# Performance work log

Hardware: AMD Instinct MI355X
Metric: run time of the kernel (lower is better)

The kernel has to match this reference:

```python
import jax, jax.numpy as jnp
import numpy as np

H = 1024
S = 32768

def setup_inputs() -> dict:
    key = jax.random.key(0)
    k1, k2, k3, k4 = jax.random.split(key, 4)
    hidden = jax.random.normal(k1, (H,), dtype=jnp.float32)
    encoder_outputs = jax.random.normal(k2, (S, H), dtype=jnp.float32)
    W = jax.random.normal(k3, (H, H), dtype=jnp.float32) * (1.0 / np.sqrt(H))
    b = jax.random.normal(k4, (H,), dtype=jnp.float32) * 0.01
    return {"hidden": hidden, "encoder_outputs": encoder_outputs, "W": W, "b": b}

def reference(hidden, encoder_outputs, W, b):
    # energy_i = dot(hidden, W @ enc_i + b); vectorized over the seq dim.
    # [S,H] @ [H,H]^T -> [S,H]; then contract with hidden -> [S]
    energies = jnp.einsum('sh,h->s', encoder_outputs @ W.T + b, hidden)
    attn = jax.nn.softmax(energies)  # softmax over seq_len (dim 0), as in F.softmax
    return attn[None, None, :]  # [1, 1, S]
```

## Files before the change

### kernel.cpp

```cpp
#include <hip/hip_runtime.h>
#include <math.h>


#define H 1024
#define S 32768

__global__ __launch_bounds__(256) void k1_v_partial(const float* __restrict__ W,
                                                    const float* __restrict__ h,
                                                    float* __restrict__ partial_v) {
    __shared__ float lds[128];
    int ic   = blockIdx.x >> 3;
    int tile = blockIdx.x & 7;
    int t    = threadIdx.x;
    int c    = tile * 128 + (t & 127);
    int par  = t >> 7;
    int j0   = ic * 64 + par;
    float acc = 0.f;
    #pragma unroll 8
    for (int i = 0; i < 32; ++i) {
        int j = j0 + 2 * i;
        acc = fmaf(W[(size_t)j * H + c], h[j], acc);
    }
    if (par) lds[t - 128] = acc;
    __syncthreads();
    if (!par) partial_v[ic * H + c] = acc + lds[t];
}

__global__ __launch_bounds__(256) void k1b_v_reduce(const float* __restrict__ partial_v,
                                                    float* __restrict__ v) {
    int k = blockIdx.x * 256 + threadIdx.x;
    float acc = 0.f;
    #pragma unroll
    for (int ic = 0; ic < 16; ++ic)
        acc += partial_v[ic * H + k];
    v[k] = acc;
}

__global__ __launch_bounds__(256) void k2_energies(const float* __restrict__ E,
                                                   const float* __restrict__ v,
                                                   float* __restrict__ energies,
                                                   float* __restrict__ bmax) {
    __shared__ float vl[H];
    __shared__ float red[8];
    int t = threadIdx.x;

    ((float4*)vl)[t] = ((const float4*)v)[t];
    __syncthreads();

    int wave = t >> 6, lane = t & 63;
    size_t row0 = (size_t)blockIdx.x * 8 + wave * 2;
    const float4* e0 = (const float4*)(E + row0 * H);
    const float4* e1 = (const float4*)(E + (row0 + 1) * H);
    const float4* v4 = (const float4*)vl;

    float a0 = 0.f, a1 = 0.f;
    #pragma unroll
    for (int p = 0; p < 4; ++p) {
        float4 vv = v4[p * 64 + lane];
        float4 x0 = e0[p * 64 + lane];
        float4 x1 = e1[p * 64 + lane];
        a0 += x0.x * vv.x + x0.y * vv.y + x0.z * vv.z + x0.w * vv.w;
        a1 += x1.x * vv.x + x1.y * vv.y + x1.z * vv.z + x1.w * vv.w;
    }
    #pragma unroll
    for (int off = 32; off; off >>= 1) {
        a0 += __shfl_down(a0, off, 64);
        a1 += __shfl_down(a1, off, 64);
    }
    if (lane == 0) {
        energies[row0]     = a0;
        energies[row0 + 1] = a1;
        red[wave * 2]      = a0;
        red[wave * 2 + 1]  = a1;
    }
    __syncthreads();
    if (t == 0) {
        float m = fmaxf(fmaxf(red[0], red[1]), fmaxf(red[2], red[3]));
        m = fmaxf(m, fmaxf(fmaxf(red[4], red[5]), fmaxf(red[6], red[7])));
        bmax[blockIdx.x] = m;
    }
}

__global__ __launch_bounds__(256) void k3_exp(float* __restrict__ out,
                                              const float* __restrict__ bmax,
                                              float* __restrict__ psum) {
    __shared__ float lds[8];
    int tid = threadIdx.x, lane = tid & 63, wave = tid >> 6;

    float m = -INFINITY;
    #pragma unroll 4
    for (int i = tid; i < 4096; i += 256)
        m = fmaxf(m, bmax[i]);
    #pragma unroll
    for (int off = 32; off; off >>= 1)
        m = fmaxf(m, __shfl_down(m, off, 64));
    if (lane == 0) lds[wave] = m;
    __syncthreads();
    float gmax = fmaxf(fmaxf(lds[0], lds[1]), fmaxf(lds[2], lds[3]));

    int s = blockIdx.x * 256 + tid;
    float p = __expf(out[s] - gmax);
    out[s] = p;

    float a = p;
    #pragma unroll
    for (int off = 32; off; off >>= 1)
        a += __shfl_down(a, off, 64);
    if (lane == 0) lds[4 + wave] = a;
    __syncthreads();
    if (tid == 0)
        psum[blockIdx.x] = (lds[4] + lds[5]) + (lds[6] + lds[7]);
}

__global__ __launch_bounds__(256) void k4_norm(float* __restrict__ out,
                                               const float* __restrict__ psum) {
    __shared__ float lds[4];
    int tid = threadIdx.x, lane = tid & 63, wave = tid >> 6;

    float a = (tid < 128) ? psum[tid] : 0.f;
    #pragma unroll
    for (int off = 32; off; off >>= 1)
        a += __shfl_down(a, off, 64);
    if (lane == 0) lds[wave] = a;
    __syncthreads();
    float inv = 1.f / ((lds[0] + lds[1]) + (lds[2] + lds[3]));

    int s = blockIdx.x * 256 + tid;
    out[s] *= inv;
}

extern "C" void kernel_launch(void* const* d_in, const int* in_sizes, int n_in,
                              void* d_out, int out_size, void* d_ws, size_t ws_size,
                              hipStream_t stream) {
    const float* h = (const float*)d_in[0];
    const float* E = (const float*)d_in[1];
    const float* W = (const float*)d_in[2];
    float* out = (float*)d_out;
    float* ws  = (float*)d_ws;

    float* partial_v = ws;
    float* v         = ws + 16 * 1024;
    float* bmax      = ws + 17 * 1024;
    float* psum      = ws + 17 * 1024 + 4096;

    k1_v_partial<<<128,  256, 0, stream>>>(W, h, partial_v);
    k1b_v_reduce<<<4,    256, 0, stream>>>(partial_v, v);
    k2_energies <<<4096, 256, 0, stream>>>(E, v, out, bmax);
    k3_exp      <<<128,  256, 0, stream>>>(out, bmax, psum);
    k4_norm     <<<128,  256, 0, stream>>>(out, psum);
}
```

Before: 39.26 us.

## Fuse softmax exp and normalize via grid barrier; widen energy kernel rows per wave

The exp and normalize kernels are merged into one kernel. An agent-scope atomic counter acts as a grid barrier, so each thread keeps its exp value in a register instead of writing it out and reading it back, and one launch goes away. The energies kernel now handles 4 rows per wave and holds v in registers instead of LDS, with per-wave max values and no block-level sync. The barrier relies on all 128 blocks being resident at once, and the counter is reset by an earlier kernel, which adds an ordering dependency between launches.

```diff
diff --git a/kernel.cpp b/kernel.cpp
--- a/kernel.cpp
+++ b/kernel.cpp
@@ -27,69 +27,72 @@
 }
 
 __global__ __launch_bounds__(256) void k1b_v_reduce(const float* __restrict__ partial_v,
-                                                    float* __restrict__ v) {
+                                                    float* __restrict__ v,
+                                                    unsigned int* __restrict__ ctr) {
     int k = blockIdx.x * 256 + threadIdx.x;
     float acc = 0.f;
     #pragma unroll
     for (int ic = 0; ic < 16; ++ic)
         acc += partial_v[ic * H + k];
     v[k] = acc;
+    if (blockIdx.x == 0 && threadIdx.x == 0) *ctr = 0u;
 }
 
 __global__ __launch_bounds__(256) void k2_energies(const float* __restrict__ E,
                                                    const float* __restrict__ v,
                                                    float* __restrict__ energies,
                                                    float* __restrict__ bmax) {
-    __shared__ float vl[H];
-    __shared__ float red[8];
-    int t = threadIdx.x;
+    int t = threadIdx.x, wave = t >> 6, lane = t & 63;
 
-    ((float4*)vl)[t] = ((const float4*)v)[t];
-    __syncthreads();
+    const float4* V4 = (const float4*)v;
+    float4 vr0 = V4[lane];
+    float4 vr1 = V4[64 + lane];
+    float4 vr2 = V4[128 + lane];
+    float4 vr3 = V4[192 + lane];
 
-    int wave = t >> 6, lane = t & 63;
-    size_t row0 = (size_t)blockIdx.x * 8 + wave * 2;
-    const float4* e0 = (const float4*)(E + row0 * H);
-    const float4* e1 = (const float4*)(E + (row0 + 1) * H);
-    const float4* v4 = (const float4*)vl;
+    size_t row0 = (size_t)blockIdx.x * 16 + wave * 4;
+    const float4* R0 = (const float4*)(E + row0 * H);
+    const float4* R1 = R0 + 256;
+    const float4* R2 = R0 + 512;
+    const float4* R3 = R0 + 768;
 
-    float a0 = 0.f, a1 = 0.f;
+    float a0 = 0.f, a1 = 0.f, a2 = 0.f, a3 = 0.f;
     #pragma unroll
     for (int p = 0; p < 4; ++p) {
-        float4 vv = v4[p * 64 + lane];
-        float4 x0 = e0[p * 64 + lane];
-        float4 x1 = e1[p * 64 + lane];
+        int idx = p * 64 + lane;
+        float4 x0 = R0[idx];
+        float4 x1 = R1[idx];
+        float4 x2 = R2[idx];
+        float4 x3 = R3[idx];
+        float4 vv = (p == 0) ? vr0 : (p == 1) ? vr1 : (p == 2) ? vr2 : vr3;
         a0 += x0.x * vv.x + x0.y * vv.y + x0.z * vv.z + x0.w * vv.w;
         a1 += x1.x * vv.x + x1.y * vv.y + x1.z * vv.z + x1.w * vv.w;
+        a2 += x2.x * vv.x + x2.y * vv.y + x2.z * vv.z + x2.w * vv.w;
+        a3 += x3.x * vv.x + x3.y * vv.y + x3.z * vv.z + x3.w * vv.w;
     }
     #pragma unroll
     for (int off = 32; off; off >>= 1) {
         a0 += __shfl_down(a0, off, 64);
         a1 += __shfl_down(a1, off, 64);
+        a2 += __shfl_down(a2, off, 64);
+        a3 += __shfl_down(a3, off, 64);
     }
     if (lane == 0) {
-        energies[row0]     = a0;
-        energies[row0 + 1] = a1;
-        red[wave * 2]      = a0;
-        red[wave * 2 + 1]  = a1;
-    }
-    __syncthreads();
-    if (t == 0) {
-        float m = fmaxf(fmaxf(red[0], red[1]), fmaxf(red[2], red[3]));
-        m = fmaxf(m, fmaxf(fmaxf(red[4], red[5]), fmaxf(red[6], red[7])));
-        bmax[blockIdx.x] = m;
+        *(float4*)(energies + row0) = make_float4(a0, a1, a2, a3);
+        bmax[blockIdx.x * 4 + wave] = fmaxf(fmaxf(a0, a1), fmaxf(a2, a3));
     }
 }
 
-__global__ __launch_bounds__(256) void k3_exp(float* __restrict__ out,
-                                              const float* __restrict__ bmax,
-                                              float* __restrict__ psum) {
+__global__ __launch_bounds__(256) void k3_softmax(float* __restrict__ out,
+                                                  const float* __restrict__ bmax,
+                                                  float* __restrict__ psum,
+                                                  unsigned int* __restrict__ ctr) {
     __shared__ float lds[8];
     int tid = threadIdx.x, lane = tid & 63, wave = tid >> 6;
 
     float m = -INFINITY;
-    #pragma unroll 4
-    for (int i = tid; i < 4096; i += 256)
+    #pragma unroll 8
+    for (int i = tid; i < 8192; i += 256)
         m = fmaxf(m, bmax[i]);
     #pragma unroll
     for (int off = 32; off; off >>= 1)
@@ -100,7 +103,6 @@
 
     int s = blockIdx.x * 256 + tid;
     float p = __expf(out[s] - gmax);
-    out[s] = p;
 
     float a = p;
     #pragma unroll
@@ -108,25 +110,25 @@
         a += __shfl_down(a, off, 64);
     if (lane == 0) lds[4 + wave] = a;
     __syncthreads();
-    if (tid == 0)
+
+    if (tid == 0) {
         psum[blockIdx.x] = (lds[4] + lds[5]) + (lds[6] + lds[7]);
-}
+        __hip_atomic_fetch_add(ctr, 1u, __ATOMIC_RELEASE, __HIP_MEMORY_SCOPE_AGENT);
+        while (__hip_atomic_load(ctr, __ATOMIC_ACQUIRE, __HIP_MEMORY_SCOPE_AGENT) < 128u) {}
+    }
+    __syncthreads();
 
-__global__ __launch_bounds__(256) void k4_norm(float* __restrict__ out,
-                                               const float* __restrict__ psum) {
-    __shared__ float lds[4];
-    int tid = threadIdx.x, lane = tid & 63, wave = tid >> 6;
-
-    float a = (tid < 128) ? psum[tid] : 0.f;
+    float q = (tid < 128)
+            ? __hip_atomic_load(&psum[tid], __ATOMIC_RELAXED, __HIP_MEMORY_SCOPE_AGENT)
+            : 0.f;
     #pragma unroll
     for (int off = 32; off; off >>= 1)
-        a += __shfl_down(a, off, 64);
-    if (lane == 0) lds[wave] = a;
+        q += __shfl_down(q, off, 64);
+    if (lane == 0) lds[wave] = q;
     __syncthreads();
     float inv = 1.f / ((lds[0] + lds[1]) + (lds[2] + lds[3]));
 
-    int s = blockIdx.x * 256 + tid;
-    out[s] *= inv;
+    out[s] = p * inv;
 }
 
 extern "C" void kernel_launch(void* const* d_in, const int* in_sizes, int n_in,
@@ -138,14 +140,14 @@
     float* out = (float*)d_out;
     float* ws  = (float*)d_ws;
 
-    float* partial_v = ws;
-    float* v         = ws + 16 * 1024;
-    float* bmax      = ws + 17 * 1024;
-    float* psum      = ws + 17 * 1024 + 4096;
+    float* partial_v  = ws;
+    float* v          = ws + 16 * 1024;
+    float* bmax       = ws + 17 * 1024;
+    float* psum       = ws + 17 * 1024 + 8192;
+    unsigned int* ctr = (unsigned int*)(ws + 17 * 1024 + 8192 + 128);
 
     k1_v_partial<<<128,  256, 0, stream>>>(W, h, partial_v);
-    k1b_v_reduce<<<4,    256, 0, stream>>>(partial_v, v);
-    k2_energies <<<4096, 256, 0, stream>>>(E, v, out, bmax);
-    k3_exp      <<<128,  256, 0, stream>>>(out, bmax, psum);
-    k4_norm     <<<128,  256, 0, stream>>>(out, psum);
+    k1b_v_reduce<<<4,    256, 0, stream>>>(partial_v, v, ctr);
+    k2_energies <<<2048, 256, 0, stream>>>(E, v, out, bmax);
+    k3_softmax  <<<128,  256, 0, stream>>>(out, bmax, psum, ctr);
 }
```

New measurement: 53.73 us. +36.9%, slower.
